# Optimization experiments

Hardware: AMD Instinct MI355X
Metric: run time of the kernel (lower is better)

## Reference

```python
import jax, jax.numpy as jnp
import numpy as np

B, T_E, T_D, H = 32, 128, 128, 256  # batch, encoder len, decoder len, hidden


def lstm_scan(x, h0, c0, Wih, Whh, bih, bhh):
    """Single-layer PyTorch-style LSTM over x: [B, T, F] -> (hs, cs) each [T, B, H]."""
    bias = bih + bhh

    def step(carry, xt):
        h, c = carry
        gates = xt @ Wih.T + h @ Whh.T + bias  # [B, 4H], gate order i,f,g,o
        i, f, g, o = jnp.split(gates, 4, axis=-1)
        i = jax.nn.sigmoid(i)
        f = jax.nn.sigmoid(f)
        o = jax.nn.sigmoid(o)
        g = jnp.tanh(g)
        c = f * c + i * g
        h = o * jnp.tanh(c)
        return (h, c), (h, c)

    _, (hs, cs) = jax.lax.scan(step, (h0, c0), jnp.swapaxes(x, 0, 1))
    return hs, cs


def setup_inputs() -> dict:
    key = jax.random.key(0)
    ks = jax.random.split(key, 16)
    seq = jax.random.normal(ks[0], (B, T_E), jnp.float32)
    seq_m = jax.random.randint(ks[1], (B, 1), 1, T_E + 1)  # valid lengths in [1, T_E]
    pos = jnp.arange(T_E)[None, :]
    seq = jnp.where(pos < seq_m, seq, 0.0)  # zero-pad beyond length (drives the mask)
    target = jax.random.normal(ks[2], (B, T_D), jnp.float32)

    s = 0.1
    nrm = lambda k, shape: s * jax.random.normal(k, shape, jnp.float32)
    return dict(
        seq=seq, seq_m=seq_m, target=target,
        Wih_e=nrm(ks[3], (4 * H, 1)), Whh_e=nrm(ks[4], (4 * H, H)),
        bih_e=nrm(ks[5], (4 * H,)), bhh_e=nrm(ks[6], (4 * H,)),
        Wih_d=nrm(ks[7], (4 * H, 1)), Whh_d=nrm(ks[8], (4 * H, H)),
        bih_d=nrm(ks[9], (4 * H,)), bhh_d=nrm(ks[10], (4 * H,)),
        We=nrm(ks[11], (H, H)), be=nrm(ks[12], (H,)),
        Wd=nrm(ks[13], (H, H)), bd=nrm(ks[14], (H,)),
        v=jnp.ones((H,), jnp.float32),
    )


def reference(seq, seq_m, target,
              Wih_e, Whh_e, bih_e, bhh_e,
              Wih_d, Whh_d, bih_d, bhh_d,
              We, be, Wd, bd, v):
    zeros = jnp.zeros((B, H), seq.dtype)
    # Encoder: one fused scan instead of the original per-timestep Python loop
    hs_e, cs_e = lstm_scan(seq[..., None], zeros, zeros, Wih_e, Whh_e, bih_e, bhh_e)
    e = jnp.swapaxes(hs_e, 0, 1)  # [B, T_E, H]

    # Grab encoder state at the last valid step (seq_m - 1) per batch element
    last = seq_m[:, 0] - 1  # [B]
    bidx = jnp.arange(B)
    e_hs = hs_e[last, bidx]  # [B, H]
    e_cs = cs_e[last, bidx]

    # Decoder initialized from the selected encoder state
    hs_d, _ = lstm_scan(target[..., None], e_hs, e_cs, Wih_d, Whh_d, bih_d, bhh_d)
    d = jnp.swapaxes(hs_d, 0, 1)  # [B, T_D, H]

    e2 = e @ We.T + be  # [B, T_E, H]
    d2 = d @ Wd.T + bd  # [B, T_D, H]

    # Additive (Bahdanau) attention: tanh(e_j + d_i) . v  -> [B, T_D, T_E]
    t = jnp.tanh(d2[:, :, None, :] + e2[:, None, :, :])  # [B, T_D, T_E, H]
    p = jnp.einsum('bijh,h->bij', t, v)

    # Masking: original sets seq[:,0]=0.1 then adds 1000 where seq value nonzero,
    # after subtracting 1000 everywhere -> padded (zero) positions end up at -1000.
    seq0 = seq.at[:, 0].set(0.1)
    mask = (seq0 != 0).astype(p.dtype)  # [B, T_E]
    p = p + (mask[:, None, :] - 1.0) * 1000.0

    return jax.nn.softmax(p, axis=-1)  # pointer distribution over encoder positions
```

## Files before the change

kernel.cpp:

```cpp
#include <hip/hip_runtime.h>
#include <hip/hip_bf16.h>

#define BB 32
#define TT 128
#define HH 256
#define G4 4
#define UPB 64
#define RPB 256

#define AGENT __HIP_MEMORY_SCOPE_AGENT
#define AL(p) __hip_atomic_load((p), __ATOMIC_RELAXED, AGENT)

__device__ __forceinline__ float sigmoid_f(float x) {
    return 1.f / (1.f + __expf(-x));
}
__device__ __forceinline__ float tanh_f(float x) {
    float e = __expf(2.f * x);
    return 1.f - 2.f / (e + 1.f);
}

__global__ __launch_bounds__(256) void prep_transpose(
    const float* __restrict__ We, const float* __restrict__ Wd,
    float* __restrict__ WeT, float* __restrict__ WdT) {
    __shared__ float t[64][65];
    const int m = blockIdx.x >> 4;
    const int tile = blockIdx.x & 15;
    const float* S = m ? Wd : We;
    float* D = m ? WdT : WeT;
    const int r0 = (tile >> 2) * 64, c0 = (tile & 3) * 64;
    const int lr = threadIdx.x >> 4;
    const int lc = threadIdx.x & 15;
    for (int rr = lr; rr < 64; rr += 16)
        *(float4*)&t[rr][lc * 4] = *(const float4*)&S[(r0 + rr) * HH + c0 + lc * 4];
    __syncthreads();
    for (int rr = lr; rr < 64; rr += 16) {
        float4 v;
        v.x = t[lc * 4 + 0][rr];
        v.y = t[lc * 4 + 1][rr];
        v.z = t[lc * 4 + 2][rr];
        v.w = t[lc * 4 + 3][rr];
        *(float4*)&D[(c0 + rr) * HH + r0 + lc * 4] = v;
    }
}

__global__ __launch_bounds__(512, 2) void lstm_kernel(
    const float* __restrict__ seq,
    const int* __restrict__ seq_m,
    const float* __restrict__ target,
    const float* __restrict__ Wih_e,
    const float* __restrict__ Whh_e,
    const float* __restrict__ bih_e, const float* __restrict__ bhh_e,
    const float* __restrict__ Wih_d, const float* __restrict__ Whh_d,
    const float* __restrict__ bih_d, const float* __restrict__ bhh_d,
    float* __restrict__ e_out,
    float* __restrict__ d_out,
    unsigned long long* __restrict__ mbox,
    unsigned long long* __restrict__ hsave)
{
    const int blk = blockIdx.x;
    const int b = blk & 31;
    const int g = blk >> 5;
    const int tid = threadIdx.x;
    const int row_local = tid >> 1;
    const int half = tid & 1;
    const int gate = row_local >> 6;
    const int u_local = row_local & 63;
    const int row_global = gate * HH + g * UPB + u_local;
    const int last = seq_m[b] - 1;

    __shared__ float h_lds[HH];
    __shared__ float g_lds[RPB];
    __shared__ float x_lds[2 * TT];

    for (int i = tid; i < TT; i += 512) {
        x_lds[i] = seq[b * TT + i];
        x_lds[TT + i] = target[b * TT + i];
    }

    float4 w[32];
    float bias_r, wih_r;
    auto loadw = [&](const float* Whh, const float* Wih,
                     const float* bih, const float* bhh) {
        const float4* wr = (const float4*)(Whh + row_global * HH + half * 128);
#pragma unroll
        for (int i = 0; i < 32; ++i) w[i] = wr[i];
        bias_r = bih[row_global] + bhh[row_global];
        wih_r = Wih[row_global];
    };
    loadw(Whh_e, Wih_e, bih_e, bhh_e);

    if (tid < 64) ((float4*)h_lds)[tid] = make_float4(0.f, 0.f, 0.f, 0.f);
    __syncthreads();

    float c = 0.f, c_saved = 0.f, h_saved = 0.f;

    for (int t = 0; t < 2 * TT; ++t) {
        const int phase = t >> 7;
        const int tt = t & 127;
        const float x = x_lds[t];

        const float4* h4 = ((const float4*)h_lds) + half * 32;
        float4 a4 = make_float4(0.f, 0.f, 0.f, 0.f);
#pragma unroll
        for (int i = 0; i < 32; ++i) {
            float4 hv = h4[i];
            a4.x = fmaf(w[i].x, hv.x, a4.x);
            a4.y = fmaf(w[i].y, hv.y, a4.y);
            a4.z = fmaf(w[i].z, hv.z, a4.z);
            a4.w = fmaf(w[i].w, hv.w, a4.w);
        }
        float acc = (a4.x + a4.y) + (a4.z + a4.w);
        acc += __shfl_xor(acc, 1);
        float gv = acc + bias_r + x * wih_r;
        if (half == 0) g_lds[row_local] = gv;
        __syncthreads();

        if (tid < 64) {
            float gi = g_lds[tid];
            float gf = g_lds[64 + tid];
            float gg = g_lds[128 + tid];
            float go = g_lds[192 + tid];
            float si = sigmoid_f(gi);
            float sf = sigmoid_f(gf);
            float tg = tanh_f(gg);
            float so = sigmoid_f(go);
            c = sf * c + si * tg;
            float h = so * tanh_f(c);
            const int ug = g * UPB + tid;
            unsigned long long pkt =
                ((unsigned long long)(unsigned)(t + 1) << 32) | __float_as_uint(h);
            __hip_atomic_store(&mbox[(t & 1) * BB * HH + b * HH + ug], pkt,
                               __ATOMIC_RELAXED, AGENT);
            if (phase == 0 && tt == last) {
                c_saved = c;
                h_saved = h;
                unsigned long long spkt =
                    (1ull << 32) | (unsigned long long)__float_as_uint(h);
                __hip_atomic_store(&hsave[b * HH + ug], spkt, __ATOMIC_RELAXED, AGENT);
            }
            h_lds[ug] = (t == TT - 1) ? h_saved : h;
            (phase ? d_out : e_out)[(b * TT + tt) * HH + ug] = h;
        }

        if (tid >= 64 && tid < 256) {
            const int p = (g + (tid >> 6)) & 3;
            const int lane = tid & 63;
            const int pu = p * UPB + lane;
            unsigned long long* src;
            unsigned want;
            if (t == TT - 1) {
                src = &hsave[b * HH + pu];
                want = 1u;
            } else {
                src = &mbox[(t & 1) * BB * HH + b * HH + pu];
                want = (unsigned)(t + 1);
            }
            unsigned long long pv;
            {
                unsigned long long r0 = AL(src);
                __builtin_amdgcn_s_sleep(3);
                unsigned long long r1 = AL(src);
                __builtin_amdgcn_s_sleep(3);
                unsigned long long r2 = AL(src);
                __builtin_amdgcn_s_sleep(3);
                unsigned long long r3 = AL(src);
                for (;;) {
                    if ((unsigned)(r0 >> 32) == want) { pv = r0; break; }
                    r0 = AL(src);
                    if ((unsigned)(r1 >> 32) == want) { pv = r1; break; }
                    r1 = AL(src);
                    if ((unsigned)(r2 >> 32) == want) { pv = r2; break; }
                    r2 = AL(src);
                    if ((unsigned)(r3 >> 32) == want) { pv = r3; break; }
                    r3 = AL(src);
                }
            }
            h_lds[pu] = __uint_as_float((unsigned)pv);
        }
        __syncthreads();

        if (t == TT - 1) {
            loadw(Whh_d, Wih_d, bih_d, bhh_d);
            c = c_saved;
        }
    }
}

__global__ __launch_bounds__(256) void proj_kernel(
    const float* __restrict__ e_in, const float* __restrict__ d_in,
    const float* __restrict__ WeT, const float* __restrict__ WdT,
    const float* __restrict__ be, const float* __restrict__ bd,
    float* __restrict__ e2, float* __restrict__ d2) {
    __shared__ float tile[16][HH];
    const int blk = blockIdx.x;
    const bool isd = blk >= 256;
    const float* in = isd ? d_in : e_in;
    const float* WT = isd ? WdT : WeT;
    const float* bias = isd ? bd : be;
    float* out = isd ? d2 : e2;
    const int r0 = (isd ? blk - 256 : blk) * 16;
    const int tid = threadIdx.x;

    {
        const float4* src = (const float4*)(in + r0 * HH);
        float4* dst = (float4*)(&tile[0][0]);
        for (int idx = tid; idx < 16 * 64; idx += 256) dst[idx] = src[idx];
    }
    __syncthreads();

    float acc[16];
#pragma unroll
    for (int r = 0; r < 16; ++r) acc[r] = 0.f;
    const int cidx = tid;
    for (int k = 0; k < HH; k += 4) {
        float w0 = WT[(k + 0) * HH + cidx];
        float w1 = WT[(k + 1) * HH + cidx];
        float w2 = WT[(k + 2) * HH + cidx];
        float w3 = WT[(k + 3) * HH + cidx];
#pragma unroll
        for (int r = 0; r < 16; ++r) {
            float4 iv = *(const float4*)&tile[r][k];
            acc[r] = fmaf(iv.x, w0, acc[r]);
            acc[r] = fmaf(iv.y, w1, acc[r]);
            acc[r] = fmaf(iv.z, w2, acc[r]);
            acc[r] = fmaf(iv.w, w3, acc[r]);
        }
    }
    const float bb = bias[cidx];
#pragma unroll
    for (int r = 0; r < 16; ++r) out[(r0 + r) * HH + cidx] = acc[r] + bb;
}

#define EPAD 260
__global__ __launch_bounds__(256) void attn_kernel(
    const float* __restrict__ e2, const float* __restrict__ d2,
    const float* __restrict__ vv, const float* __restrict__ seq,
    float* __restrict__ out) {
    __shared__ float e2c[32][EPAD];
    __shared__ float d2t[8][EPAD];
    __shared__ float p_lds[8][128];
    __shared__ float v_lds[HH];

    const int blk = blockIdx.x;
    const int b = blk >> 4;
    const int i0 = (blk & 15) * 8;
    const int tid = threadIdx.x;
    const int jl = tid & 31, ii = tid >> 5;

    if (tid < 64) *(float4*)&v_lds[tid * 4] = ((const float4*)vv)[tid];
    for (int idx = tid; idx < 8 * 64; idx += 256) {
        int r = idx >> 6, q = idx & 63;
        *(float4*)&d2t[r][q * 4] = ((const float4*)(d2 + (b * TT + i0 + r) * HH))[q];
    }

    for (int jc = 0; jc < TT; jc += 32) {
        __syncthreads();
        for (int idx = tid; idx < 32 * 64; idx += 256) {
            int r = idx >> 6, q = idx & 63;
            *(float4*)&e2c[r][q * 4] = ((const float4*)(e2 + (b * TT + jc + r) * HH))[q];
        }
        __syncthreads();

        float acc = 0.f;
        for (int h = 0; h < HH; h += 4) {
            float4 ev = *(const float4*)&e2c[jl][h];
            float4 dv = *(const float4*)&d2t[ii][h];
            float4 vx = *(const float4*)&v_lds[h];
            acc = fmaf(tanh_f(ev.x + dv.x), vx.x, acc);
            acc = fmaf(tanh_f(ev.y + dv.y), vx.y, acc);
            acc = fmaf(tanh_f(ev.z + dv.z), vx.z, acc);
            acc = fmaf(tanh_f(ev.w + dv.w), vx.w, acc);
        }
        const int j = jc + jl;
        float sv = (j == 0) ? 0.1f : seq[b * TT + j];
        if (sv == 0.f) acc -= 1000.f;
        p_lds[ii][j] = acc;
    }
    __syncthreads();

    const int gr = tid >> 5, l = tid & 31;
    float x0 = p_lds[gr][l], x1 = p_lds[gr][l + 32];
    float x2 = p_lds[gr][l + 64], x3 = p_lds[gr][l + 96];
    float m = fmaxf(fmaxf(x0, x1), fmaxf(x2, x3));
#pragma unroll
    for (int o = 16; o >= 1; o >>= 1) m = fmaxf(m, __shfl_xor(m, o));
    float q0 = __expf(x0 - m), q1 = __expf(x1 - m);
    float q2 = __expf(x2 - m), q3 = __expf(x3 - m);
    float s = (q0 + q1) + (q2 + q3);
#pragma unroll
    for (int o = 16; o >= 1; o >>= 1) s += __shfl_xor(s, o);
    float inv = 1.f / s;
    float* orow = out + (b * TT + i0 + gr) * TT;
    orow[l] = q0 * inv;
    orow[l + 32] = q1 * inv;
    orow[l + 64] = q2 * inv;
    orow[l + 96] = q3 * inv;
}

extern "C" void kernel_launch(void* const* d_in, const int* in_sizes, int n_in,
                              void* d_out, int out_size, void* d_ws, size_t ws_size,
                              hipStream_t stream) {
    const float* seq = (const float*)d_in[0];
    const int* seq_m = (const int*)d_in[1];
    const float* target = (const float*)d_in[2];
    const float* Wih_e = (const float*)d_in[3];
    const float* Whh_e = (const float*)d_in[4];
    const float* bih_e = (const float*)d_in[5];
    const float* bhh_e = (const float*)d_in[6];
    const float* Wih_d = (const float*)d_in[7];
    const float* Whh_d = (const float*)d_in[8];
    const float* bih_d = (const float*)d_in[9];
    const float* bhh_d = (const float*)d_in[10];
    const float* We = (const float*)d_in[11];
    const float* be = (const float*)d_in[12];
    const float* Wd = (const float*)d_in[13];
    const float* bd = (const float*)d_in[14];
    const float* vv = (const float*)d_in[15];

    float* ws = (float*)d_ws;
    const size_t SZ_ED = (size_t)BB * TT * HH;
    float* e_buf = ws;
    float* d_buf = e_buf + SZ_ED;
    float* e2 = d_buf + SZ_ED;
    float* d2 = e2 + SZ_ED;
    float* WeT = d2 + SZ_ED;
    float* WdT = WeT + HH * HH;
    unsigned long long* mbox = (unsigned long long*)(WdT + HH * HH);
    unsigned long long* hsave = mbox + 2 * BB * HH;

    const size_t needed = (4 * SZ_ED + 2 * HH * HH) * sizeof(float) +
                          3 * BB * HH * sizeof(unsigned long long);
    if (ws_size < needed) return;

    hipMemsetAsync(mbox, 0, 3 * BB * HH * sizeof(unsigned long long), stream);
    prep_transpose<<<32, 256, 0, stream>>>(We, Wd, WeT, WdT);
    lstm_kernel<<<BB * G4, 512, 0, stream>>>(seq, seq_m, target, Wih_e, Whh_e, bih_e,
                                             bhh_e, Wih_d, Whh_d, bih_d, bhh_d, e_buf,
                                             d_buf, mbox, hsave);
    proj_kernel<<<512, 256, 0, stream>>>(e_buf, d_buf, WeT, WdT, be, bd, e2, d2);
    attn_kernel<<<512, 256, 0, stream>>>(e2, d2, vv, seq, (float*)d_out);
}
```

Before: 671.5 us.

## Split LSTM matvec halves by wave, enlarge attention decoder tile, use fast reciprocal

In the LSTM kernel, the two halves of each row's dot product now go to separate waves instead of adjacent lanes. The partial sums are combined through LDS by the gate-activation threads, which removes the shuffle, and bias and input weights move from registers into LDS. The attention kernel now processes 32 decoder rows per block (4 per thread) so each e2 chunk load is reused across more rows, with padded p storage and an 8-lane softmax. Sigmoid and tanh use the hardware reciprocal in place of division. The risks are the attention grid shrinking from 512 to 128 blocks, which lowers parallelism, and the larger LDS footprint.

Result: slower. 695.6 us (+3.6%).

```diff
diff --git a/kernel.cpp b/kernel.cpp
--- a/kernel.cpp
+++ b/kernel.cpp
@@ -11,12 +11,13 @@
 #define AGENT __HIP_MEMORY_SCOPE_AGENT
 #define AL(p) __hip_atomic_load((p), __ATOMIC_RELAXED, AGENT)
 
+__device__ __forceinline__ float rcp_f(float x) { return __builtin_amdgcn_rcpf(x); }
 __device__ __forceinline__ float sigmoid_f(float x) {
-    return 1.f / (1.f + __expf(-x));
+    return rcp_f(1.f + __expf(-x));
 }
 __device__ __forceinline__ float tanh_f(float x) {
     float e = __expf(2.f * x);
-    return 1.f - 2.f / (e + 1.f);
+    return 1.f - 2.f * rcp_f(e + 1.f);
 }
 
 __global__ __launch_bounds__(256) void prep_transpose(
@@ -61,15 +62,19 @@
     const int b = blk & 31;
     const int g = blk >> 5;
     const int tid = threadIdx.x;
-    const int row_local = tid >> 1;
-    const int half = tid & 1;
-    const int gate = row_local >> 6;
-    const int u_local = row_local & 63;
+    const int wave = tid >> 6;
+    const int lane = tid & 63;
+    const int half = wave & 1;
+    const int row = (wave >> 1) * 64 + lane;
+    const int gate = row >> 6;
+    const int u_local = row & 63;
     const int row_global = gate * HH + g * UPB + u_local;
     const int last = seq_m[b] - 1;
 
     __shared__ float h_lds[HH];
-    __shared__ float g_lds[RPB];
+    __shared__ float g_lds[2 * RPB];
+    __shared__ float bias_lds[RPB];
+    __shared__ float wih_lds[RPB];
     __shared__ float x_lds[2 * TT];
 
     for (int i = tid; i < TT; i += 512) {
@@ -78,14 +83,15 @@
     }
 
     float4 w[32];
-    float bias_r, wih_r;
     auto loadw = [&](const float* Whh, const float* Wih,
                      const float* bih, const float* bhh) {
         const float4* wr = (const float4*)(Whh + row_global * HH + half * 128);
 #pragma unroll
         for (int i = 0; i < 32; ++i) w[i] = wr[i];
-        bias_r = bih[row_global] + bhh[row_global];
-        wih_r = Wih[row_global];
+        if (half == 0) {
+            bias_lds[row] = bih[row_global] + bhh[row_global];
+            wih_lds[row] = Wih[row_global];
+        }
     };
     loadw(Whh_e, Wih_e, bih_e, bhh_e);
 
@@ -97,9 +103,8 @@
     for (int t = 0; t < 2 * TT; ++t) {
         const int phase = t >> 7;
         const int tt = t & 127;
-        const float x = x_lds[t];
-
-        const float4* h4 = ((const float4*)h_lds) + half * 32;
+
+        const float4* h4 = (const float4*)(h_lds + (half << 7));
         float4 a4 = make_float4(0.f, 0.f, 0.f, 0.f);
 #pragma unroll
         for (int i = 0; i < 32; ++i) {
@@ -109,17 +114,19 @@
             a4.z = fmaf(w[i].z, hv.z, a4.z);
             a4.w = fmaf(w[i].w, hv.w, a4.w);
         }
-        float acc = (a4.x + a4.y) + (a4.z + a4.w);
-        acc += __shfl_xor(acc, 1);
-        float gv = acc + bias_r + x * wih_r;
-        if (half == 0) g_lds[row_local] = gv;
+        g_lds[(half << 8) + row] = (a4.x + a4.y) + (a4.z + a4.w);
         __syncthreads();
 
         if (tid < 64) {
-            float gi = g_lds[tid];
-            float gf = g_lds[64 + tid];
-            float gg = g_lds[128 + tid];
-            float go = g_lds[192 + tid];
+            const float x = x_lds[t];
+            float gi = g_lds[tid] + g_lds[256 + tid] + bias_lds[tid] +
+                       x * wih_lds[tid];
+            float gf = g_lds[64 + tid] + g_lds[320 + tid] + bias_lds[64 + tid] +
+                       x * wih_lds[64 + tid];
+            float gg = g_lds[128 + tid] + g_lds[384 + tid] + bias_lds[128 + tid] +
+                       x * wih_lds[128 + tid];
+            float go = g_lds[192 + tid] + g_lds[448 + tid] + bias_lds[192 + tid] +
+                       x * wih_lds[192 + tid];
             float si = sigmoid_f(gi);
             float sf = sigmoid_f(gf);
             float tg = tanh_f(gg);
@@ -144,8 +151,8 @@
 
         if (tid >= 64 && tid < 256) {
             const int p = (g + (tid >> 6)) & 3;
-            const int lane = tid & 63;
-            const int pu = p * UPB + lane;
+            const int pl = tid & 63;
+            const int pu = p * UPB + pl;
             unsigned long long* src;
             unsigned want;
             if (t == TT - 1) {
@@ -232,23 +239,24 @@
 }
 
 #define EPAD 260
+#define PPAD 132
 __global__ __launch_bounds__(256) void attn_kernel(
     const float* __restrict__ e2, const float* __restrict__ d2,
     const float* __restrict__ vv, const float* __restrict__ seq,
     float* __restrict__ out) {
     __shared__ float e2c[32][EPAD];
-    __shared__ float d2t[8][EPAD];
-    __shared__ float p_lds[8][128];
+    __shared__ float d2t[32][EPAD];
+    __shared__ float p_lds[32][PPAD];
     __shared__ float v_lds[HH];
 
     const int blk = blockIdx.x;
-    const int b = blk >> 4;
-    const int i0 = (blk & 15) * 8;
+    const int b = blk >> 2;
+    const int i0 = (blk & 3) * 32;
     const int tid = threadIdx.x;
-    const int jl = tid & 31, ii = tid >> 5;
+    const int jl = tid & 31, ig = tid >> 5;
 
     if (tid < 64) *(float4*)&v_lds[tid * 4] = ((const float4*)vv)[tid];
-    for (int idx = tid; idx < 8 * 64; idx += 256) {
+    for (int idx = tid; idx < 32 * 64; idx += 256) {
         int r = idx >> 6, q = idx & 63;
         *(float4*)&d2t[r][q * 4] = ((const float4*)(d2 + (b * TT + i0 + r) * HH))[q];
     }
@@ -261,40 +269,63 @@
         }
         __syncthreads();
 
-        float acc = 0.f;
+        float a0 = 0.f, a1 = 0.f, a2 = 0.f, a3 = 0.f;
         for (int h = 0; h < HH; h += 4) {
             float4 ev = *(const float4*)&e2c[jl][h];
-            float4 dv = *(const float4*)&d2t[ii][h];
             float4 vx = *(const float4*)&v_lds[h];
-            acc = fmaf(tanh_f(ev.x + dv.x), vx.x, acc);
-            acc = fmaf(tanh_f(ev.y + dv.y), vx.y, acc);
-            acc = fmaf(tanh_f(ev.z + dv.z), vx.z, acc);
-            acc = fmaf(tanh_f(ev.w + dv.w), vx.w, acc);
+            float4 d0 = *(const float4*)&d2t[ig * 4 + 0][h];
+            float4 d1 = *(const float4*)&d2t[ig * 4 + 1][h];
+            float4 d2v = *(const float4*)&d2t[ig * 4 + 2][h];
+            float4 d3 = *(const float4*)&d2t[ig * 4 + 3][h];
+            a0 = fmaf(tanh_f(ev.x + d0.x), vx.x, a0);
+            a0 = fmaf(tanh_f(ev.y + d0.y), vx.y, a0);
+            a0 = fmaf(tanh_f(ev.z + d0.z), vx.z, a0);
+            a0 = fmaf(tanh_f(ev.w + d0.w), vx.w, a0);
+            a1 = fmaf(tanh_f(ev.x + d1.x), vx.x, a1);
+            a1 = fmaf(tanh_f(ev.y + d1.y), vx.y, a1);
+            a1 = fmaf(tanh_f(ev.z + d1.z), vx.z, a1);
+            a1 = fmaf(tanh_f(ev.w + d1.w), vx.w, a1);
+            a2 = fmaf(tanh_f(ev.x + d2v.x), vx.x, a2);
+            a2 = fmaf(tanh_f(ev.y + d2v.y), vx.y, a2);
+            a2 = fmaf(tanh_f(ev.z + d2v.z), vx.z, a2);
+            a2 = fmaf(tanh_f(ev.w + d2v.w), vx.w, a2);
+            a3 = fmaf(tanh_f(ev.x + d3.x), vx.x, a3);
+            a3 = fmaf(tanh_f(ev.y + d3.y), vx.y, a3);
+            a3 = fmaf(tanh_f(ev.z + d3.z), vx.z, a3);
+            a3 = fmaf(tanh_f(ev.w + d3.w), vx.w, a3);
         }
         const int j = jc + jl;
         float sv = (j == 0) ? 0.1f : seq[b * TT + j];
-        if (sv == 0.f) acc -= 1000.f;
-        p_lds[ii][j] = acc;
+        float msk = (sv == 0.f) ? -1000.f : 0.f;
+        p_lds[ig * 4 + 0][j] = a0 + msk;
+        p_lds[ig * 4 + 1][j] = a1 + msk;
+        p_lds[ig * 4 + 2][j] = a2 + msk;
+        p_lds[ig * 4 + 3][j] = a3 + msk;
     }
     __syncthreads();
 
-    const int gr = tid >> 5, l = tid & 31;
-    float x0 = p_lds[gr][l], x1 = p_lds[gr][l + 32];
-    float x2 = p_lds[gr][l + 64], x3 = p_lds[gr][l + 96];
-    float m = fmaxf(fmaxf(x0, x1), fmaxf(x2, x3));
-#pragma unroll
-    for (int o = 16; o >= 1; o >>= 1) m = fmaxf(m, __shfl_xor(m, o));
-    float q0 = __expf(x0 - m), q1 = __expf(x1 - m);
-    float q2 = __expf(x2 - m), q3 = __expf(x3 - m);
-    float s = (q0 + q1) + (q2 + q3);
-#pragma unroll
-    for (int o = 16; o >= 1; o >>= 1) s += __shfl_xor(s, o);
-    float inv = 1.f / s;
-    float* orow = out + (b * TT + i0 + gr) * TT;
-    orow[l] = q0 * inv;
-    orow[l + 32] = q1 * inv;
-    orow[l + 64] = q2 * inv;
-    orow[l + 96] = q3 * inv;
+    const int r = tid >> 3, l8 = tid & 7;
+    float xr[16];
+    float m = -1e30f;
+#pragma unroll
+    for (int k = 0; k < 16; ++k) {
+        xr[k] = p_lds[r][l8 + 8 * k];
+        m = fmaxf(m, xr[k]);
+    }
+#pragma unroll
+    for (int o = 4; o >= 1; o >>= 1) m = fmaxf(m, __shfl_xor(m, o));
+    float s = 0.f;
+#pragma unroll
+    for (int k = 0; k < 16; ++k) {
+        xr[k] = __expf(xr[k] - m);
+        s += xr[k];
+    }
+#pragma unroll
+    for (int o = 4; o >= 1; o >>= 1) s += __shfl_xor(s, o);
+    float inv = rcp_f(s);
+    float* orow = out + (b * TT + i0 + r) * TT;
+#pragma unroll
+    for (int k = 0; k < 16; ++k) orow[l8 + 8 * k] = xr[k] * inv;
 }
 
 extern "C" void kernel_launch(void* const* d_in, const int* in_sizes, int n_in,
@@ -338,5 +369,5 @@
                                              bhh_e, Wih_d, Whh_d, bih_d, bhh_d, e_buf,
                                              d_buf, mbox, hsave);
     proj_kernel<<<512, 256, 0, stream>>>(e_buf, d_buf, WeT, WdT, be, bd, e2, d2);
-    attn_kernel<<<512, 256, 0, stream>>>(e2, d2, vv, seq, (float*)d_out);
-}
+    attn_kernel<<<BB * 4, 256, 0, stream>>>(e2, d2, vv, seq, (float*)d_out);
+}
```
